# Kernel optimization log

Hardware: AMD Instinct MI355X
Metric: run time of the kernel (lower is better)

The kernel has to match this reference:

```python
import jax, jax.numpy as jnp
import numpy as np


def _rconv(x, w, b):
    # reflection-pad 1 then 3x3 valid conv (same spatial size), NCHW/OIHW
    xp = jnp.pad(x, ((0, 0), (0, 0), (1, 1), (1, 1)), mode='reflect')
    y = jax.lax.conv_general_dilated(
        xp, w, window_strides=(1, 1), padding='VALID',
        dimension_numbers=('NCHW', 'OIHW', 'NCHW'))
    return y + b[None, :, None, None]


def setup_inputs() -> dict:
    key = jax.random.key(0)
    ks = jax.random.split(key, 12)
    B, C, H, W = 4, 256, 64, 64
    IC = 128  # inter_channels
    s = lambda fan_in: 1.0 / np.sqrt(fan_in)
    return {
        'query_feat': jax.random.normal(ks[0], (B, C, H, W), jnp.float32),
        'key_feat': jax.random.normal(ks[1], (B, C, H, W), jnp.float32),
        # 1x1 conv projections (stored as [out, in])
        'w_theta': jax.random.normal(ks[2], (IC, C), jnp.float32) * s(C),
        'b_theta': jnp.zeros((IC,), jnp.float32),
        'w_phi': jax.random.normal(ks[3], (IC, C), jnp.float32) * s(C),
        'b_phi': jnp.zeros((IC,), jnp.float32),
        # post-correlation block: conv(1->32), residual(32), conv(32->1)
        'w_in': jax.random.normal(ks[4], (32, 1, 3, 3), jnp.float32) * s(9),
        'b_in': jnp.zeros((32,), jnp.float32),
        'w_r1': jax.random.normal(ks[5], (32, 32, 3, 3), jnp.float32) * s(32 * 9),
        'b_r1': jnp.zeros((32,), jnp.float32),
        'w_r2': jax.random.normal(ks[6], (32, 32, 3, 3), jnp.float32) * s(32 * 9),
        'b_r2': jnp.zeros((32,), jnp.float32),
        'w_out': jax.random.normal(ks[7], (1, 32, 3, 3), jnp.float32) * s(32 * 9),
        'b_out': jnp.zeros((1,), jnp.float32),
    }


def reference(query_feat, key_feat, w_theta, b_theta, w_phi, b_phi,
              w_in, b_in, w_r1, b_r1, w_r2, b_r2, w_out, b_out):
    B, C, H, W = query_feat.shape
    N = H * W
    # 1x1 conv projections, flattened to sequences
    theta = jnp.einsum('oc,bchw->bohw', w_theta, query_feat) + b_theta[None, :, None, None]
    phi = jnp.einsum('oc,bchw->bohw', w_phi, key_feat) + b_phi[None, :, None, None]
    theta = theta.reshape(B, -1, N).transpose(0, 2, 1)  # [B, N, IC]
    phi = phi.reshape(B, -1, N)                          # [B, IC, N]
    # correlation matrix [B, N, N] then max over key positions
    f = jnp.matmul(theta, phi)
    sim = jnp.max(f, axis=-1).reshape(B, 1, H, W)
    # post-correlation conv refinement
    h = _rconv(sim, w_in, b_in)                      # 1 -> 32
    r = jax.nn.relu(_rconv(h, w_r1, b_r1))           # residual block
    r = _rconv(r, w_r2, b_r2)
    h = h + r
    out = _rconv(h, w_out, b_out)                    # 32 -> 1
    return out
```

## Files before the change

### kernel.cpp

```cpp
#include <hip/hip_runtime.h>

#define B_ 4
#define C_ 256
#define HH 64
#define WW 64
#define N_ 4096
#define IC_ 128
#define JC_ 8

typedef __attribute__((ext_vector_type(8))) short bf16x8;
typedef __attribute__((ext_vector_type(4))) float f32x4;

__device__ __forceinline__ short f2bf(float f) {
    unsigned u = __builtin_bit_cast(unsigned, f);
    unsigned r = (u + 0x7FFFu + ((u >> 16) & 1u)) >> 16;
    return (short)r;
}

__device__ __forceinline__ int refl(int v) {
    return v < 0 ? -v : (v > 63 ? 126 - v : v);
}

__global__ __launch_bounds__(256) void k_cvt_w(const float* __restrict__ wt,
                                               const float* __restrict__ wp,
                                               short* __restrict__ wtb,
                                               short* __restrict__ wpb) {
    int i = blockIdx.x * 256 + threadIdx.x;
    wtb[i] = f2bf(wt[i]);
    wpb[i] = f2bf(wp[i]);
}

__global__ __launch_bounds__(256) void k_project(
    const float* __restrict__ qf, const float* __restrict__ kf,
    const short* __restrict__ wq, const short* __restrict__ wk,
    const float* __restrict__ bq, const float* __restrict__ bk,
    short* __restrict__ outq, short* __restrict__ outk) {
    int z = blockIdx.z;
    const float* x = z ? kf : qf;
    const short* wbf = z ? wk : wq;
    const float* bias = z ? bk : bq;
    short* outT = z ? outk : outq;

    int b = blockIdx.y;
    int n0 = blockIdx.x * 32;
    int t = threadIdx.x;
    int lane = t & 63, wv = t >> 6;
    int l15 = lane & 15, q4 = lane >> 4;
    const float* xb = x + (size_t)b * C_ * N_;

    __shared__ float xs[2][32][36];

    f32x4 acc[2][2];
#pragma unroll
    for (int rf = 0; rf < 2; rf++)
#pragma unroll
        for (int cfi = 0; cfi < 2; cfi++) acc[rf][cfi] = (f32x4){0.f, 0.f, 0.f, 0.f};

    int sr = t >> 3, sc = t & 7;
    *(f32x4*)(&xs[0][sr][sc * 4]) = *(const f32x4*)(xb + (size_t)sr * N_ + n0 + sc * 4);

    for (int ks = 0; ks < 8; ks++) {
        __syncthreads();
        int buf = ks & 1;
        if (ks < 7) {
            int cb = (ks + 1) * 32;
            *(f32x4*)(&xs[buf ^ 1][sr][sc * 4]) =
                *(const f32x4*)(xb + (size_t)(cb + sr) * N_ + n0 + sc * 4);
        }
        int cbase = ks * 32 + q4 * 8;
        bf16x8 a[2];
#pragma unroll
        for (int rf = 0; rf < 2; rf++)
#pragma unroll
            for (int j = 0; j < 8; j++) a[rf][j] = f2bf(xs[buf][q4 * 8 + j][rf * 16 + l15]);
#pragma unroll
        for (int cfi = 0; cfi < 2; cfi++) {
            int cf = wv * 2 + cfi;
            bf16x8 bfr = *(const bf16x8*)(wbf + (size_t)(cf * 16 + l15) * C_ + cbase);
#pragma unroll
            for (int rf = 0; rf < 2; rf++)
                acc[rf][cfi] = __builtin_amdgcn_mfma_f32_16x16x32_bf16(a[rf], bfr, acc[rf][cfi], 0, 0, 0);
        }
    }
#pragma unroll
    for (int cfi = 0; cfi < 2; cfi++) {
        int ic = (wv * 2 + cfi) * 16 + l15;
        float bv = bias[ic];
#pragma unroll
        for (int rf = 0; rf < 2; rf++) {
#pragma unroll
            for (int r = 0; r < 4; r++) {
                int n = n0 + rf * 16 + q4 * 4 + r;
                outT[((size_t)b * N_ + n) * IC_ + ic] = f2bf(acc[rf][cfi][r] + bv);
            }
        }
    }
}

__global__ __launch_bounds__(256, 4) void k_corr(const short* __restrict__ thetaT,
                                                 const short* __restrict__ phiT,
                                                 float* __restrict__ simp) {
    __shared__ short ph[2][64][136];

    int b = blockIdx.z, jc = blockIdx.y;
    int i0 = blockIdx.x * 128;
    int t = threadIdx.x;
    int lane = t & 63, w = t >> 6;
    int l15 = lane & 15, q4 = lane >> 4;

    const short* thb = thetaT + ((size_t)b * N_ + i0 + w * 32) * IC_;
    const short* phb = phiT + ((size_t)b * N_ + jc * (N_ / JC_)) * IC_;

    bf16x8 afr[2][4];
#pragma unroll
    for (int rf = 0; rf < 2; rf++)
#pragma unroll
        for (int ks = 0; ks < 4; ks++)
            afr[rf][ks] = *(const bf16x8*)(thb + (size_t)(rf * 16 + l15) * IC_ + ks * 32 + q4 * 8);

    int srow = t >> 4, sc8 = t & 15;
#pragma unroll
    for (int k = 0; k < 4; k++)
        *(bf16x8*)(&ph[0][srow + k * 16][sc8 * 8]) =
            *(const bf16x8*)(phb + (size_t)(srow + k * 16) * IC_ + sc8 * 8);

    f32x4 rmax[2];
#pragma unroll
    for (int rf = 0; rf < 2; rf++) rmax[rf] = (f32x4){-3.0e38f, -3.0e38f, -3.0e38f, -3.0e38f};

    const int NT = (N_ / JC_) / 64;
    for (int it = 0; it < NT; it++) {
        int buf = it & 1;
        __syncthreads();
        if (it < NT - 1) {
            int j0 = (it + 1) * 64;
#pragma unroll
            for (int k = 0; k < 4; k++)
                *(bf16x8*)(&ph[buf ^ 1][srow + k * 16][sc8 * 8]) =
                    *(const bf16x8*)(phb + (size_t)(j0 + srow + k * 16) * IC_ + sc8 * 8);
        }
#pragma unroll
        for (int jf = 0; jf < 4; jf++) {
            bf16x8 bfr[4];
#pragma unroll
            for (int ks = 0; ks < 4; ks++)
                bfr[ks] = *(const bf16x8*)(&ph[buf][jf * 16 + l15][ks * 32 + q4 * 8]);
#pragma unroll
            for (int rf = 0; rf < 2; rf++) {
                f32x4 a2 = (f32x4){0.f, 0.f, 0.f, 0.f};
#pragma unroll
                for (int ks = 0; ks < 4; ks++)
                    a2 = __builtin_amdgcn_mfma_f32_16x16x32_bf16(afr[rf][ks], bfr[ks], a2, 0, 0, 0);
#pragma unroll
                for (int r = 0; r < 4; r++) rmax[rf][r] = fmaxf(rmax[rf][r], a2[r]);
            }
        }
    }

#pragma unroll
    for (int rf = 0; rf < 2; rf++) {
#pragma unroll
        for (int r = 0; r < 4; r++) {
            float v = rmax[rf][r];
            v = fmaxf(v, __shfl_xor(v, 1));
            v = fmaxf(v, __shfl_xor(v, 2));
            v = fmaxf(v, __shfl_xor(v, 4));
            v = fmaxf(v, __shfl_xor(v, 8));
            rmax[rf][r] = v;
        }
    }
    if (l15 == 0) {
        float* sp = simp + ((size_t)(b * JC_ + jc)) * N_ + i0 + w * 32;
#pragma unroll
        for (int rf = 0; rf < 2; rf++)
#pragma unroll
            for (int r = 0; r < 4; r++) sp[rf * 16 + q4 * 4 + r] = rmax[rf][r];
    }
}

__global__ __launch_bounds__(256) void k_conv_in(const float* __restrict__ simp,
                                                 const float* __restrict__ w,
                                                 const float* __restrict__ bias,
                                                 float* __restrict__ h) {
    int y = blockIdx.x, b = blockIdx.y;
    int t = threadIdx.x;
    int oc = t >> 3, x8 = t & 7;
    __shared__ float srow[3][66];
    const float* sb = simp + (size_t)b * JC_ * N_;
    if (t < 192) {
        int r = t >> 6, x = t & 63;
        int idx = refl(y - 1 + r) * 64 + x;
        float v = -3.0e38f;
#pragma unroll
        for (int jc = 0; jc < JC_; jc++) v = fmaxf(v, sb[jc * N_ + idx]);
        srow[r][x + 1] = v;
    }
    if (t < 3) {
        int gy = refl(y - 1 + t);
        float vl = -3.0e38f, vr = -3.0e38f;
#pragma unroll
        for (int jc = 0; jc < JC_; jc++) {
            vl = fmaxf(vl, sb[jc * N_ + gy * 64 + 1]);
            vr = fmaxf(vr, sb[jc * N_ + gy * 64 + 62]);
        }
        srow[t][0] = vl;
        srow[t][65] = vr;
    }
    __syncthreads();

    float wr[9];
#pragma unroll
    for (int k = 0; k < 9; k++) wr[k] = w[oc * 9 + k];
    float bv = bias[oc];
    float acc[8];
#pragma unroll
    for (int xi = 0; xi < 8; xi++) acc[xi] = bv;
#pragma unroll
    for (int ky = 0; ky < 3; ky++)
#pragma unroll
        for (int kx = 0; kx < 3; kx++) {
            float wv2 = wr[ky * 3 + kx];
#pragma unroll
            for (int xi = 0; xi < 8; xi++) acc[xi] += wv2 * srow[ky][x8 * 8 + xi + kx];
        }
    float* op = h + (((size_t)b * 32 + oc) * 64 + y) * 64 + x8 * 8;
#pragma unroll
    for (int xi = 0; xi < 8; xi++) op[xi] = acc[xi];
}

template <bool RELU, bool ADD>
__global__ __launch_bounds__(256) void k_conv_r(const float* __restrict__ in,
                                                const float* __restrict__ w,
                                                const float* __restrict__ bias,
                                                float* __restrict__ out,
                                                const float* __restrict__ add) {
    int y = blockIdx.x, b = blockIdx.z;
    int oc0 = blockIdx.y * 16;
    int t = threadIdx.x;
    __shared__ float tile[32][3][68];
    __shared__ float wlds[32 * 16 * 12];

#pragma unroll
    for (int k = 0; k < 18; k++) {
        int id = t + k * 256;
        int ocl = id / 288;
        int rem = id - ocl * 288;
        int ic = rem / 9;
        int tap = rem - ic * 9;
        wlds[(ic * 16 + ocl) * 12 + tap] = w[(size_t)(oc0 + ocl) * 288 + rem];
    }

#pragma unroll
    for (int r = 0; r < 3; r++) {
        int gy = refl(y - 1 + r);
#pragma unroll
        for (int i = 0; i < 2; i++) {
            int idx = t + i * 256;
            int ic = idx >> 4, c4 = idx & 15;
            f32x4 v = *(const f32x4*)(in + (((size_t)b * 32 + ic) * 64 + gy) * 64 + c4 * 4);
#pragma unroll
            for (int s = 0; s < 4; s++) tile[ic][r][c4 * 4 + s + 1] = v[s];
        }
    }
    if (t < 96) {
        int ic = t / 3, r = t - ic * 3;
        int gy = refl(y - 1 + r);
        const float* row = in + (((size_t)b * 32 + ic) * 64 + gy) * 64;
        tile[ic][r][0] = row[1];
        tile[ic][r][65] = row[62];
    }
    __syncthreads();

    int ocl = t >> 4, x4 = (t & 15) * 4;
    float bv = bias[oc0 + ocl];
    float acc[4];
#pragma unroll
    for (int xi = 0; xi < 4; xi++) acc[xi] = bv;

#pragma unroll 2
    for (int ic = 0; ic < 32; ic++) {
        const float* wr = &wlds[(ic * 16 + ocl) * 12];
        f32x4 W0 = *(const f32x4*)(wr);
        f32x4 W1 = *(const f32x4*)(wr + 4);
        f32x4 W2 = *(const f32x4*)(wr + 8);
        float w0 = W0[0], w1 = W0[1], w2 = W0[2], w3 = W0[3];
        float w4 = W1[0], w5 = W1[1], w6 = W1[2], w7 = W1[3];
        float w8 = W2[0];
        float xr[3][8];
#pragma unroll
        for (int r = 0; r < 3; r++) {
            const float* rowp = &tile[ic][r][x4];
            f32x4 A = *(const f32x4*)(rowp);
            f32x4 Bv = *(const f32x4*)(rowp + 4);
            xr[r][0] = A[0]; xr[r][1] = A[1]; xr[r][2] = A[2]; xr[r][3] = A[3];
            xr[r][4] = Bv[0]; xr[r][5] = Bv[1]; xr[r][6] = Bv[2]; xr[r][7] = Bv[3];
        }
#pragma unroll
        for (int xi = 0; xi < 4; xi++) {
            acc[xi] += w0 * xr[0][xi] + w1 * xr[0][xi + 1] + w2 * xr[0][xi + 2] +
                       w3 * xr[1][xi] + w4 * xr[1][xi + 1] + w5 * xr[1][xi + 2] +
                       w6 * xr[2][xi] + w7 * xr[2][xi + 1] + w8 * xr[2][xi + 2];
        }
    }
    size_t off = (((size_t)b * 32 + oc0 + ocl) * 64 + y) * 64 + x4;
#pragma unroll
    for (int xi = 0; xi < 4; xi++) {
        float v = acc[xi];
        if (RELU) v = fmaxf(v, 0.f);
        if (ADD) v += add[off + xi];
        out[off + xi] = v;
    }
}

__global__ __launch_bounds__(256) void k_conv_out(const float* __restrict__ hb,
                                                  const float* __restrict__ w,
                                                  const float* __restrict__ bias,
                                                  float* __restrict__ outp) {
    int y = blockIdx.x, b = blockIdx.y;
    int t = threadIdx.x;
    int x = t & 63, g = t >> 6;
    __shared__ float red[4][64];
    __shared__ float wl[288];
    for (int k = t; k < 288; k += 256) wl[k] = w[k];
    __syncthreads();
    float acc = 0.f;
#pragma unroll
    for (int i = 0; i < 8; i++) {
        int ic = g * 8 + i;
        const float* wp = wl + ic * 9;
#pragma unroll
        for (int ky = 0; ky < 3; ky++) {
            int gy = refl(y + ky - 1);
            const float* row = hb + (((size_t)b * 32 + ic) * 64 + gy) * 64;
#pragma unroll
            for (int kx = 0; kx < 3; kx++) {
                int gx = refl(x + kx - 1);
                acc += wp[ky * 3 + kx] * row[gx];
            }
        }
    }
    red[g][x] = acc;
    __syncthreads();
    if (t < 64) {
        outp[((size_t)b * 64 + y) * 64 + x] =
            bias[0] + red[0][t] + red[1][t] + red[2][t] + red[3][t];
    }
}

extern "C" void kernel_launch(void* const* d_in, const int* in_sizes, int n_in,
                              void* d_out, int out_size, void* d_ws, size_t ws_size,
                              hipStream_t stream) {
    const float* q = (const float*)d_in[0];
    const float* kf = (const float*)d_in[1];
    const float* w_theta = (const float*)d_in[2];
    const float* b_theta = (const float*)d_in[3];
    const float* w_phi = (const float*)d_in[4];
    const float* b_phi = (const float*)d_in[5];
    const float* w_in = (const float*)d_in[6];
    const float* b_in = (const float*)d_in[7];
    const float* w_r1 = (const float*)d_in[8];
    const float* b_r1 = (const float*)d_in[9];
    const float* w_r2 = (const float*)d_in[10];
    const float* b_r2 = (const float*)d_in[11];
    const float* w_out = (const float*)d_in[12];
    const float* b_out = (const float*)d_in[13];
    float* out = (float*)d_out;

    char* ws = (char*)d_ws;
    short* thetaT = (short*)(ws);
    short* phiT = (short*)(ws + 4194304);
    short* wthb = (short*)(ws + 8388608);
    short* wphb = (short*)(ws + 8454144);
    float* simp = (float*)(ws + 8519680);
    float* h = (float*)(ws);
    float* r = (float*)(ws + 2097152);

    k_cvt_w<<<128, 256, 0, stream>>>(w_theta, w_phi, wthb, wphb);
    k_project<<<dim3(128, 4, 2), 256, 0, stream>>>(q, kf, wthb, wphb, b_theta, b_phi,
                                                   thetaT, phiT);
    k_corr<<<dim3(32, JC_, 4), 256, 0, stream>>>(thetaT, phiT, simp);
    k_conv_in<<<dim3(64, 4), 256, 0, stream>>>(simp, w_in, b_in, h);
    k_conv_r<true, false><<<dim3(64, 2, 4), 256, 0, stream>>>(h, w_r1, b_r1, r, nullptr);
    k_conv_r<false, true><<<dim3(64, 2, 4), 256, 0, stream>>>(r, w_r2, b_r2, h, h);
    k_conv_out<<<dim3(64, 4), 256, 0, stream>>>(h, w_out, b_out, out);
}
```

Before: 166.9 us.

## Fuse weight conversion and conv_in into neighbors; double rows per corr block

Drops the separate weight bf16 conversion kernel: the projection kernel now reads fp32 weights and rounds them in registers. The correlation kernel handles 256 query rows per block instead of 128, so each LDS phi tile feeds twice as many MFMAs, at the cost of more registers (launch bound lowered to 2) and half as many blocks. The first 1->32 conv is fused into the first residual conv: each block recomputes h over a 3-row halo from the partial-max buffer, and one y-slice of blocks writes h out. Two launches go away in exchange for some redundant conv_in work.

```diff
diff --git a/kernel.cpp b/kernel.cpp
--- a/kernel.cpp
+++ b/kernel.cpp
@@ -21,23 +21,14 @@
     return v < 0 ? -v : (v > 63 ? 126 - v : v);
 }
 
-__global__ __launch_bounds__(256) void k_cvt_w(const float* __restrict__ wt,
-                                               const float* __restrict__ wp,
-                                               short* __restrict__ wtb,
-                                               short* __restrict__ wpb) {
-    int i = blockIdx.x * 256 + threadIdx.x;
-    wtb[i] = f2bf(wt[i]);
-    wpb[i] = f2bf(wp[i]);
-}
-
 __global__ __launch_bounds__(256) void k_project(
     const float* __restrict__ qf, const float* __restrict__ kf,
-    const short* __restrict__ wq, const short* __restrict__ wk,
+    const float* __restrict__ wq, const float* __restrict__ wk,
     const float* __restrict__ bq, const float* __restrict__ bk,
     short* __restrict__ outq, short* __restrict__ outk) {
     int z = blockIdx.z;
     const float* x = z ? kf : qf;
-    const short* wbf = z ? wk : wq;
+    const float* wf = z ? wk : wq;
     const float* bias = z ? bk : bq;
     short* outT = z ? outk : outq;
 
@@ -76,7 +67,15 @@
 #pragma unroll
         for (int cfi = 0; cfi < 2; cfi++) {
             int cf = wv * 2 + cfi;
-            bf16x8 bfr = *(const bf16x8*)(wbf + (size_t)(cf * 16 + l15) * C_ + cbase);
+            const float* wrow = wf + (size_t)(cf * 16 + l15) * C_ + cbase;
+            f32x4 w0 = *(const f32x4*)(wrow);
+            f32x4 w1 = *(const f32x4*)(wrow + 4);
+            bf16x8 bfr;
+#pragma unroll
+            for (int j = 0; j < 4; j++) {
+                bfr[j] = f2bf(w0[j]);
+                bfr[j + 4] = f2bf(w1[j]);
+            }
 #pragma unroll
             for (int rf = 0; rf < 2; rf++)
                 acc[rf][cfi] = __builtin_amdgcn_mfma_f32_16x16x32_bf16(a[rf], bfr, acc[rf][cfi], 0, 0, 0);
@@ -97,36 +96,36 @@
     }
 }
 
-__global__ __launch_bounds__(256, 4) void k_corr(const short* __restrict__ thetaT,
+__global__ __launch_bounds__(256, 2) void k_corr(const short* __restrict__ thetaT,
                                                  const short* __restrict__ phiT,
                                                  float* __restrict__ simp) {
     __shared__ short ph[2][64][136];
 
     int b = blockIdx.z, jc = blockIdx.y;
-    int i0 = blockIdx.x * 128;
+    int i0 = blockIdx.x * 256;
     int t = threadIdx.x;
     int lane = t & 63, w = t >> 6;
     int l15 = lane & 15, q4 = lane >> 4;
 
-    const short* thb = thetaT + ((size_t)b * N_ + i0 + w * 32) * IC_;
+    const short* thb = thetaT + ((size_t)b * N_ + i0 + w * 64) * IC_;
     const short* phb = phiT + ((size_t)b * N_ + jc * (N_ / JC_)) * IC_;
 
-    bf16x8 afr[2][4];
-#pragma unroll
-    for (int rf = 0; rf < 2; rf++)
+    bf16x8 afr[4][4];
+#pragma unroll
+    for (int rf = 0; rf < 4; rf++)
 #pragma unroll
         for (int ks = 0; ks < 4; ks++)
             afr[rf][ks] = *(const bf16x8*)(thb + (size_t)(rf * 16 + l15) * IC_ + ks * 32 + q4 * 8);
 
-    int srow = t >> 4, sc8 = t & 15;
+    int sr = t >> 4, sc8 = t & 15;
 #pragma unroll
     for (int k = 0; k < 4; k++)
-        *(bf16x8*)(&ph[0][srow + k * 16][sc8 * 8]) =
-            *(const bf16x8*)(phb + (size_t)(srow + k * 16) * IC_ + sc8 * 8);
-
-    f32x4 rmax[2];
-#pragma unroll
-    for (int rf = 0; rf < 2; rf++) rmax[rf] = (f32x4){-3.0e38f, -3.0e38f, -3.0e38f, -3.0e38f};
+        *(bf16x8*)(&ph[0][sr + k * 16][sc8 * 8]) =
+            *(const bf16x8*)(phb + (size_t)(sr + k * 16) * IC_ + sc8 * 8);
+
+    f32x4 rmax[4];
+#pragma unroll
+    for (int rf = 0; rf < 4; rf++) rmax[rf] = (f32x4){-3.0e38f, -3.0e38f, -3.0e38f, -3.0e38f};
 
     const int NT = (N_ / JC_) / 64;
     for (int it = 0; it < NT; it++) {
@@ -136,8 +135,8 @@
             int j0 = (it + 1) * 64;
 #pragma unroll
             for (int k = 0; k < 4; k++)
-                *(bf16x8*)(&ph[buf ^ 1][srow + k * 16][sc8 * 8]) =
-                    *(const bf16x8*)(phb + (size_t)(j0 + srow + k * 16) * IC_ + sc8 * 8);
+                *(bf16x8*)(&ph[buf ^ 1][sr + k * 16][sc8 * 8]) =
+                    *(const bf16x8*)(phb + (size_t)(j0 + sr + k * 16) * IC_ + sc8 * 8);
         }
 #pragma unroll
         for (int jf = 0; jf < 4; jf++) {
@@ -146,7 +145,7 @@
             for (int ks = 0; ks < 4; ks++)
                 bfr[ks] = *(const bf16x8*)(&ph[buf][jf * 16 + l15][ks * 32 + q4 * 8]);
 #pragma unroll
-            for (int rf = 0; rf < 2; rf++) {
+            for (int rf = 0; rf < 4; rf++) {
                 f32x4 a2 = (f32x4){0.f, 0.f, 0.f, 0.f};
 #pragma unroll
                 for (int ks = 0; ks < 4; ks++)
@@ -158,7 +157,7 @@
     }
 
 #pragma unroll
-    for (int rf = 0; rf < 2; rf++) {
+    for (int rf = 0; rf < 4; rf++) {
 #pragma unroll
         for (int r = 0; r < 4; r++) {
             float v = rmax[rf][r];
@@ -170,62 +169,128 @@
         }
     }
     if (l15 == 0) {
-        float* sp = simp + ((size_t)(b * JC_ + jc)) * N_ + i0 + w * 32;
-#pragma unroll
-        for (int rf = 0; rf < 2; rf++)
+        float* sp = simp + ((size_t)(b * JC_ + jc)) * N_ + i0 + w * 64;
+#pragma unroll
+        for (int rf = 0; rf < 4; rf++)
 #pragma unroll
             for (int r = 0; r < 4; r++) sp[rf * 16 + q4 * 4 + r] = rmax[rf][r];
     }
 }
 
-__global__ __launch_bounds__(256) void k_conv_in(const float* __restrict__ simp,
-                                                 const float* __restrict__ w,
-                                                 const float* __restrict__ bias,
-                                                 float* __restrict__ h) {
-    int y = blockIdx.x, b = blockIdx.y;
+__global__ __launch_bounds__(256) void k_r1_fused(
+    const float* __restrict__ simp,
+    const float* __restrict__ win, const float* __restrict__ bin,
+    const float* __restrict__ w, const float* __restrict__ bias,
+    float* __restrict__ rout, float* __restrict__ hout) {
+    int y = blockIdx.x, b = blockIdx.z;
+    int oc0 = blockIdx.y * 16;
     int t = threadIdx.x;
-    int oc = t >> 3, x8 = t & 7;
-    __shared__ float srow[3][66];
+    __shared__ float srow[5][66];
+    __shared__ float tile[32][3][68];
+    __shared__ float wlds[32 * 16 * 12];
+    __shared__ float wi[288];
+    __shared__ float bi[32];
+
+    for (int k = t; k < 288; k += 256) wi[k] = win[k];
+    if (t < 32) bi[t] = bin[t];
+
     const float* sb = simp + (size_t)b * JC_ * N_;
-    if (t < 192) {
-        int r = t >> 6, x = t & 63;
-        int idx = refl(y - 1 + r) * 64 + x;
+    for (int idx = t; idx < 330; idx += 256) {
+        int d = idx / 66, cc = idx - d * 66;
+        int row = refl(y - 2 + d);
+        int col = refl(cc - 1);
         float v = -3.0e38f;
 #pragma unroll
-        for (int jc = 0; jc < JC_; jc++) v = fmaxf(v, sb[jc * N_ + idx]);
-        srow[r][x + 1] = v;
-    }
-    if (t < 3) {
-        int gy = refl(y - 1 + t);
-        float vl = -3.0e38f, vr = -3.0e38f;
-#pragma unroll
-        for (int jc = 0; jc < JC_; jc++) {
-            vl = fmaxf(vl, sb[jc * N_ + gy * 64 + 1]);
-            vr = fmaxf(vr, sb[jc * N_ + gy * 64 + 62]);
-        }
-        srow[t][0] = vl;
-        srow[t][65] = vr;
+        for (int jc = 0; jc < JC_; jc++) v = fmaxf(v, sb[jc * N_ + row * 64 + col]);
+        srow[d][cc] = v;
+    }
+
+#pragma unroll
+    for (int k = 0; k < 18; k++) {
+        int id = t + k * 256;
+        int ocl = id / 288;
+        int rem = id - ocl * 288;
+        int ic = rem / 9;
+        int tap = rem - ic * 9;
+        wlds[(ic * 16 + ocl) * 12 + tap] = w[(size_t)(oc0 + ocl) * 288 + rem];
     }
     __syncthreads();
 
-    float wr[9];
-#pragma unroll
-    for (int k = 0; k < 9; k++) wr[k] = w[oc * 9 + k];
-    float bv = bias[oc];
-    float acc[8];
-#pragma unroll
-    for (int xi = 0; xi < 8; xi++) acc[xi] = bv;
-#pragma unroll
-    for (int ky = 0; ky < 3; ky++)
-#pragma unroll
-        for (int kx = 0; kx < 3; kx++) {
-            float wv2 = wr[ky * 3 + kx];
-#pragma unroll
-            for (int xi = 0; xi < 8; xi++) acc[xi] += wv2 * srow[ky][x8 * 8 + xi + kx];
-        }
-    float* op = h + (((size_t)b * 32 + oc) * 64 + y) * 64 + x8 * 8;
-#pragma unroll
-    for (int xi = 0; xi < 8; xi++) op[xi] = acc[xi];
+    {
+        int ic = t >> 3, xg = t & 7;
+        float bv = bi[ic];
+        float wr[9];
+#pragma unroll
+        for (int k2 = 0; k2 < 9; k2++) wr[k2] = wi[ic * 9 + k2];
+#pragma unroll
+        for (int r = 0; r < 3; r++) {
+            int gy = refl(y - 1 + r);
+            int s0 = refl(gy - 1) - y + 2;
+            int s1 = gy - y + 2;
+            int s2 = refl(gy + 1) - y + 2;
+#pragma unroll
+            for (int k2 = 0; k2 < 9; k2++) {
+                int xs = k2 * 8 + xg;
+                if (xs < 66) {
+                    int cp = refl(xs - 1);
+                    float a = bv;
+                    a += wr[0] * srow[s0][cp];
+                    a += wr[1] * srow[s0][cp + 1];
+                    a += wr[2] * srow[s0][cp + 2];
+                    a += wr[3] * srow[s1][cp];
+                    a += wr[4] * srow[s1][cp + 1];
+                    a += wr[5] * srow[s1][cp + 2];
+                    a += wr[6] * srow[s2][cp];
+                    a += wr[7] * srow[s2][cp + 1];
+                    a += wr[8] * srow[s2][cp + 2];
+                    tile[ic][r][xs] = a;
+                }
+            }
+        }
+    }
+    __syncthreads();
+
+    if (blockIdx.y == 0) {
+        for (int idx = t; idx < 2048; idx += 256) {
+            int ic = idx >> 6, x = idx & 63;
+            hout[(((size_t)b * 32 + ic) * 64 + y) * 64 + x] = tile[ic][1][x + 1];
+        }
+    }
+
+    int ocl = t >> 4, x4 = (t & 15) * 4;
+    float bv = bias[oc0 + ocl];
+    float acc[4];
+#pragma unroll
+    for (int xi = 0; xi < 4; xi++) acc[xi] = bv;
+
+#pragma unroll 2
+    for (int ic = 0; ic < 32; ic++) {
+        const float* wr = &wlds[(ic * 16 + ocl) * 12];
+        f32x4 W0 = *(const f32x4*)(wr);
+        f32x4 W1 = *(const f32x4*)(wr + 4);
+        f32x4 W2 = *(const f32x4*)(wr + 8);
+        float w0 = W0[0], w1 = W0[1], w2 = W0[2], w3 = W0[3];
+        float w4 = W1[0], w5 = W1[1], w6 = W1[2], w7 = W1[3];
+        float w8 = W2[0];
+        float xr[3][8];
+#pragma unroll
+        for (int r = 0; r < 3; r++) {
+            const float* rowp = &tile[ic][r][x4];
+            f32x4 A = *(const f32x4*)(rowp);
+            f32x4 Bv = *(const f32x4*)(rowp + 4);
+            xr[r][0] = A[0]; xr[r][1] = A[1]; xr[r][2] = A[2]; xr[r][3] = A[3];
+            xr[r][4] = Bv[0]; xr[r][5] = Bv[1]; xr[r][6] = Bv[2]; xr[r][7] = Bv[3];
+        }
+#pragma unroll
+        for (int xi = 0; xi < 4; xi++) {
+            acc[xi] += w0 * xr[0][xi] + w1 * xr[0][xi + 1] + w2 * xr[0][xi + 2] +
+                       w3 * xr[1][xi] + w4 * xr[1][xi + 1] + w5 * xr[1][xi + 2] +
+                       w6 * xr[2][xi] + w7 * xr[2][xi + 1] + w8 * xr[2][xi + 2];
+        }
+    }
+    size_t off = (((size_t)b * 32 + oc0 + ocl) * 64 + y) * 64 + x4;
+#pragma unroll
+    for (int xi = 0; xi < 4; xi++) rout[off + xi] = fmaxf(acc[xi], 0.f);
 }
 
 template <bool RELU, bool ADD>
@@ -369,18 +434,14 @@
     char* ws = (char*)d_ws;
     short* thetaT = (short*)(ws);
     short* phiT = (short*)(ws + 4194304);
-    short* wthb = (short*)(ws + 8388608);
-    short* wphb = (short*)(ws + 8454144);
     float* simp = (float*)(ws + 8519680);
     float* h = (float*)(ws);
     float* r = (float*)(ws + 2097152);
 
-    k_cvt_w<<<128, 256, 0, stream>>>(w_theta, w_phi, wthb, wphb);
-    k_project<<<dim3(128, 4, 2), 256, 0, stream>>>(q, kf, wthb, wphb, b_theta, b_phi,
+    k_project<<<dim3(128, 4, 2), 256, 0, stream>>>(q, kf, w_theta, w_phi, b_theta, b_phi,
                                                    thetaT, phiT);
-    k_corr<<<dim3(32, JC_, 4), 256, 0, stream>>>(thetaT, phiT, simp);
-    k_conv_in<<<dim3(64, 4), 256, 0, stream>>>(simp, w_in, b_in, h);
-    k_conv_r<true, false><<<dim3(64, 2, 4), 256, 0, stream>>>(h, w_r1, b_r1, r, nullptr);
+    k_corr<<<dim3(16, JC_, 4), 256, 0, stream>>>(thetaT, phiT, simp);
+    k_r1_fused<<<dim3(64, 2, 4), 256, 0, stream>>>(simp, w_in, b_in, w_r1, b_r1, r, h);
     k_conv_r<false, true><<<dim3(64, 2, 4), 256, 0, stream>>>(r, w_r2, b_r2, h, h);
     k_conv_out<<<dim3(64, 4), 256, 0, stream>>>(h, w_out, b_out, out);
 }
```

Measured after the change: 171.3 us. +2.6%, slower.

## Fuse post-correlation conv chain into one cooperative kernel with grid syncs

Applied to the files above, without the earlier changes.

Replaces the four separate conv launches (conv_in, two residual convs, conv_out) with a single cooperative kernel of 256 blocks that uses grid-wide syncs between stages. The aim is to remove per-launch overhead and inter-kernel gaps. It also drops the separate weight-conversion kernel and converts the projection weights to bf16 inside the projection kernel. In exchange, each block handles both output-channel halves serially, and grid.sync carries its own cost. The old launches are kept as a fallback if the cooperative launch fails.

```diff
diff --git a/kernel.cpp b/kernel.cpp
--- a/kernel.cpp
+++ b/kernel.cpp
@@ -1,4 +1,7 @@
 #include <hip/hip_runtime.h>
+#include <hip/hip_cooperative_groups.h>
+
+namespace cg = cooperative_groups;
 
 #define B_ 4
 #define C_ 256
@@ -21,23 +24,14 @@
     return v < 0 ? -v : (v > 63 ? 126 - v : v);
 }
 
-__global__ __launch_bounds__(256) void k_cvt_w(const float* __restrict__ wt,
-                                               const float* __restrict__ wp,
-                                               short* __restrict__ wtb,
-                                               short* __restrict__ wpb) {
-    int i = blockIdx.x * 256 + threadIdx.x;
-    wtb[i] = f2bf(wt[i]);
-    wpb[i] = f2bf(wp[i]);
-}
-
 __global__ __launch_bounds__(256) void k_project(
     const float* __restrict__ qf, const float* __restrict__ kf,
-    const short* __restrict__ wq, const short* __restrict__ wk,
+    const float* __restrict__ wq, const float* __restrict__ wk,
     const float* __restrict__ bq, const float* __restrict__ bk,
     short* __restrict__ outq, short* __restrict__ outk) {
     int z = blockIdx.z;
     const float* x = z ? kf : qf;
-    const short* wbf = z ? wk : wq;
+    const float* wf = z ? wk : wq;
     const float* bias = z ? bk : bq;
     short* outT = z ? outk : outq;
 
@@ -76,7 +70,15 @@
 #pragma unroll
         for (int cfi = 0; cfi < 2; cfi++) {
             int cf = wv * 2 + cfi;
-            bf16x8 bfr = *(const bf16x8*)(wbf + (size_t)(cf * 16 + l15) * C_ + cbase);
+            const float* wrow = wf + (size_t)(cf * 16 + l15) * C_ + cbase;
+            f32x4 w0 = *(const f32x4*)(wrow);
+            f32x4 w1 = *(const f32x4*)(wrow + 4);
+            bf16x8 bfr;
+#pragma unroll
+            for (int j = 0; j < 4; j++) {
+                bfr[j] = f2bf(w0[j]);
+                bfr[j + 4] = f2bf(w1[j]);
+            }
 #pragma unroll
             for (int rf = 0; rf < 2; rf++)
                 acc[rf][cfi] = __builtin_amdgcn_mfma_f32_16x16x32_bf16(a[rf], bfr, acc[rf][cfi], 0, 0, 0);
@@ -175,6 +177,204 @@
         for (int rf = 0; rf < 2; rf++)
 #pragma unroll
             for (int r = 0; r < 4; r++) sp[rf * 16 + q4 * 4 + r] = rmax[rf][r];
+    }
+}
+
+__device__ __forceinline__ void stage_tile32(const float* in, int b, int y, int t,
+                                             float (*tile)[3][68]) {
+#pragma unroll
+    for (int r = 0; r < 3; r++) {
+        int gy = refl(y - 1 + r);
+#pragma unroll
+        for (int i = 0; i < 2; i++) {
+            int idx = t + i * 256;
+            int ic = idx >> 4, c4 = idx & 15;
+            f32x4 v = *(const f32x4*)(in + (((size_t)b * 32 + ic) * 64 + gy) * 64 + c4 * 4);
+#pragma unroll
+            for (int s = 0; s < 4; s++) tile[ic][r][c4 * 4 + s + 1] = v[s];
+        }
+    }
+    if (t < 96) {
+        int ic = t / 3, r = t - ic * 3;
+        int gy = refl(y - 1 + r);
+        const float* row = in + (((size_t)b * 32 + ic) * 64 + gy) * 64;
+        tile[ic][r][0] = row[1];
+        tile[ic][r][65] = row[62];
+    }
+}
+
+__device__ __forceinline__ void load_wlds(const float* wg, int oc0, int t, float* wlds) {
+#pragma unroll
+    for (int k = 0; k < 18; k++) {
+        int id = t + k * 256;
+        int ocl = id / 288;
+        int rem = id - ocl * 288;
+        int ic = rem / 9;
+        int tap = rem - ic * 9;
+        wlds[(ic * 16 + ocl) * 12 + tap] = wg[(size_t)(oc0 + ocl) * 288 + rem];
+    }
+}
+
+template <bool RELU, bool ADD>
+__device__ __forceinline__ void conv32_compute(const float* bias, float* outp,
+                                               const float* addp, int y, int oc0, int b,
+                                               int t, const float (*tile)[3][68],
+                                               const float* wlds) {
+    int ocl = t >> 4, x4 = (t & 15) * 4;
+    float bv = bias[oc0 + ocl];
+    float acc[4];
+#pragma unroll
+    for (int xi = 0; xi < 4; xi++) acc[xi] = bv;
+
+#pragma unroll 2
+    for (int ic = 0; ic < 32; ic++) {
+        const float* wr = &wlds[(ic * 16 + ocl) * 12];
+        f32x4 W0 = *(const f32x4*)(wr);
+        f32x4 W1 = *(const f32x4*)(wr + 4);
+        f32x4 W2 = *(const f32x4*)(wr + 8);
+        float w0 = W0[0], w1 = W0[1], w2 = W0[2], w3 = W0[3];
+        float w4 = W1[0], w5 = W1[1], w6 = W1[2], w7 = W1[3];
+        float w8 = W2[0];
+        float xr[3][8];
+#pragma unroll
+        for (int r = 0; r < 3; r++) {
+            const float* rowp = &tile[ic][r][x4];
+            f32x4 A = *(const f32x4*)(rowp);
+            f32x4 Bv = *(const f32x4*)(rowp + 4);
+            xr[r][0] = A[0]; xr[r][1] = A[1]; xr[r][2] = A[2]; xr[r][3] = A[3];
+            xr[r][4] = Bv[0]; xr[r][5] = Bv[1]; xr[r][6] = Bv[2]; xr[r][7] = Bv[3];
+        }
+#pragma unroll
+        for (int xi = 0; xi < 4; xi++) {
+            acc[xi] += w0 * xr[0][xi] + w1 * xr[0][xi + 1] + w2 * xr[0][xi + 2] +
+                       w3 * xr[1][xi] + w4 * xr[1][xi + 1] + w5 * xr[1][xi + 2] +
+                       w6 * xr[2][xi] + w7 * xr[2][xi + 1] + w8 * xr[2][xi + 2];
+        }
+    }
+    size_t off = (((size_t)b * 32 + oc0 + ocl) * 64 + y) * 64 + x4;
+#pragma unroll
+    for (int xi = 0; xi < 4; xi++) {
+        float v = acc[xi];
+        if (RELU) v = fmaxf(v, 0.f);
+        if (ADD) v += addp[off + xi];
+        outp[off + xi] = v;
+    }
+}
+
+__global__ __launch_bounds__(256) void k_tail(
+    const float* __restrict__ simp,
+    const float* __restrict__ win, const float* __restrict__ bin,
+    const float* __restrict__ w1, const float* __restrict__ b1,
+    const float* __restrict__ w2, const float* __restrict__ b2,
+    const float* __restrict__ wo, const float* __restrict__ bo,
+    float* h, float* r, float* outp) {
+    cg::grid_group grid = cg::this_grid();
+    int t = threadIdx.x;
+    int bid = blockIdx.x;
+    int y = bid & 63, b = bid >> 6;
+
+    __shared__ float srow[3][66];
+    __shared__ float tile[32][3][68];
+    __shared__ float wlds[32 * 16 * 12];
+    __shared__ float wsm[288];
+    __shared__ float bsm[32];
+    __shared__ float red[4][64];
+
+    {
+        int oc = t >> 3, x8 = t & 7;
+        const float* sb = simp + (size_t)b * JC_ * N_;
+        for (int k = t; k < 288; k += 256) wsm[k] = win[k];
+        if (t < 32) bsm[t] = bin[t];
+        if (t < 192) {
+            int rr = t >> 6, x = t & 63;
+            int idx = refl(y - 1 + rr) * 64 + x;
+            float v = -3.0e38f;
+#pragma unroll
+            for (int jc = 0; jc < JC_; jc++) v = fmaxf(v, sb[jc * N_ + idx]);
+            srow[rr][x + 1] = v;
+        }
+        if (t < 3) {
+            int gy = refl(y - 1 + t);
+            float vl = -3.0e38f, vr = -3.0e38f;
+#pragma unroll
+            for (int jc = 0; jc < JC_; jc++) {
+                vl = fmaxf(vl, sb[jc * N_ + gy * 64 + 1]);
+                vr = fmaxf(vr, sb[jc * N_ + gy * 64 + 62]);
+            }
+            srow[t][0] = vl;
+            srow[t][65] = vr;
+        }
+        __syncthreads();
+        float wr[9];
+#pragma unroll
+        for (int k = 0; k < 9; k++) wr[k] = wsm[oc * 9 + k];
+        float bv = bsm[oc];
+        float acc[8];
+#pragma unroll
+        for (int xi = 0; xi < 8; xi++) acc[xi] = bv;
+#pragma unroll
+        for (int ky = 0; ky < 3; ky++)
+#pragma unroll
+            for (int kx = 0; kx < 3; kx++) {
+                float wv2 = wr[ky * 3 + kx];
+#pragma unroll
+                for (int xi = 0; xi < 8; xi++) acc[xi] += wv2 * srow[ky][x8 * 8 + xi + kx];
+            }
+        float* op = h + (((size_t)b * 32 + oc) * 64 + y) * 64 + x8 * 8;
+#pragma unroll
+        for (int xi = 0; xi < 8; xi++) op[xi] = acc[xi];
+    }
+    __threadfence();
+    grid.sync();
+
+    stage_tile32(h, b, y, t, tile);
+#pragma unroll
+    for (int oh = 0; oh < 2; oh++) {
+        load_wlds(w1, oh * 16, t, wlds);
+        __syncthreads();
+        conv32_compute<true, false>(b1, r, nullptr, y, oh * 16, b, t, tile, wlds);
+        __syncthreads();
+    }
+    __threadfence();
+    grid.sync();
+
+    stage_tile32(r, b, y, t, tile);
+#pragma unroll
+    for (int oh = 0; oh < 2; oh++) {
+        load_wlds(w2, oh * 16, t, wlds);
+        __syncthreads();
+        conv32_compute<false, true>(b2, h, h, y, oh * 16, b, t, tile, wlds);
+        __syncthreads();
+    }
+    __threadfence();
+    grid.sync();
+
+    {
+        int x = t & 63, g = t >> 6;
+        for (int k = t; k < 288; k += 256) wsm[k] = wo[k];
+        __syncthreads();
+        float acc = 0.f;
+#pragma unroll
+        for (int i = 0; i < 8; i++) {
+            int ic = g * 8 + i;
+            const float* wp = wsm + ic * 9;
+#pragma unroll
+            for (int ky = 0; ky < 3; ky++) {
+                int gy = refl(y + ky - 1);
+                const float* row = h + (((size_t)b * 32 + ic) * 64 + gy) * 64;
+#pragma unroll
+                for (int kx = 0; kx < 3; kx++) {
+                    int gx = refl(x + kx - 1);
+                    acc += wp[ky * 3 + kx] * row[gx];
+                }
+            }
+        }
+        red[g][x] = acc;
+        __syncthreads();
+        if (t < 64) {
+            outp[((size_t)b * 64 + y) * 64 + x] =
+                bo[0] + red[0][t] + red[1][t] + red[2][t] + red[3][t];
+        }
     }
 }
 
@@ -186,7 +386,9 @@
     int t = threadIdx.x;
     int oc = t >> 3, x8 = t & 7;
     __shared__ float srow[3][66];
+    __shared__ float wsm[288];
     const float* sb = simp + (size_t)b * JC_ * N_;
+    for (int k = t; k < 288; k += 256) wsm[k] = w[k];
     if (t < 192) {
         int r = t >> 6, x = t & 63;
         int idx = refl(y - 1 + r) * 64 + x;
@@ -210,7 +412,7 @@
 
     float wr[9];
 #pragma unroll
-    for (int k = 0; k < 9; k++) wr[k] = w[oc * 9 + k];
+    for (int k = 0; k < 9; k++) wr[k] = wsm[oc * 9 + k];
     float bv = bias[oc];
     float acc[8];
 #pragma unroll
@@ -239,77 +441,10 @@
     int t = threadIdx.x;
     __shared__ float tile[32][3][68];
     __shared__ float wlds[32 * 16 * 12];
-
-#pragma unroll
-    for (int k = 0; k < 18; k++) {
-        int id = t + k * 256;
-        int ocl = id / 288;
-        int rem = id - ocl * 288;
-        int ic = rem / 9;
-        int tap = rem - ic * 9;
-        wlds[(ic * 16 + ocl) * 12 + tap] = w[(size_t)(oc0 + ocl) * 288 + rem];
-    }
-
-#pragma unroll
-    for (int r = 0; r < 3; r++) {
-        int gy = refl(y - 1 + r);
-#pragma unroll
-        for (int i = 0; i < 2; i++) {
-            int idx = t + i * 256;
-            int ic = idx >> 4, c4 = idx & 15;
-            f32x4 v = *(const f32x4*)(in + (((size_t)b * 32 + ic) * 64 + gy) * 64 + c4 * 4);
-#pragma unroll
-            for (int s = 0; s < 4; s++) tile[ic][r][c4 * 4 + s + 1] = v[s];
-        }
-    }
-    if (t < 96) {
-        int ic = t / 3, r = t - ic * 3;
-        int gy = refl(y - 1 + r);
-        const float* row = in + (((size_t)b * 32 + ic) * 64 + gy) * 64;
-        tile[ic][r][0] = row[1];
-        tile[ic][r][65] = row[62];
-    }
+    load_wlds(w, oc0, t, wlds);
+    stage_tile32(in, b, y, t, tile);
     __syncthreads();
-
-    int ocl = t >> 4, x4 = (t & 15) * 4;
-    float bv = bias[oc0 + ocl];
-    float acc[4];
-#pragma unroll
-    for (int xi = 0; xi < 4; xi++) acc[xi] = bv;
-
-#pragma unroll 2
-    for (int ic = 0; ic < 32; ic++) {
-        const float* wr = &wlds[(ic * 16 + ocl) * 12];
-        f32x4 W0 = *(const f32x4*)(wr);
-        f32x4 W1 = *(const f32x4*)(wr + 4);
-        f32x4 W2 = *(const f32x4*)(wr + 8);
-        float w0 = W0[0], w1 = W0[1], w2 = W0[2], w3 = W0[3];
-        float w4 = W1[0], w5 = W1[1], w6 = W1[2], w7 = W1[3];
-        float w8 = W2[0];
-        float xr[3][8];
-#pragma unroll
-        for (int r = 0; r < 3; r++) {
-            const float* rowp = &tile[ic][r][x4];
-            f32x4 A = *(const f32x4*)(rowp);
-            f32x4 Bv = *(const f32x4*)(rowp + 4);
-            xr[r][0] = A[0]; xr[r][1] = A[1]; xr[r][2] = A[2]; xr[r][3] = A[3];
-            xr[r][4] = Bv[0]; xr[r][5] = Bv[1]; xr[r][6] = Bv[2]; xr[r][7] = Bv[3];
-        }
-#pragma unroll
-        for (int xi = 0; xi < 4; xi++) {
-            acc[xi] += w0 * xr[0][xi] + w1 * xr[0][xi + 1] + w2 * xr[0][xi + 2] +
-                       w3 * xr[1][xi] + w4 * xr[1][xi + 1] + w5 * xr[1][xi + 2] +
-                       w6 * xr[2][xi] + w7 * xr[2][xi + 1] + w8 * xr[2][xi + 2];
-        }
-    }
-    size_t off = (((size_t)b * 32 + oc0 + ocl) * 64 + y) * 64 + x4;
-#pragma unroll
-    for (int xi = 0; xi < 4; xi++) {
-        float v = acc[xi];
-        if (RELU) v = fmaxf(v, 0.f);
-        if (ADD) v += add[off + xi];
-        out[off + xi] = v;
-    }
+    conv32_compute<RELU, ADD>(bias, out, add, y, oc0, b, t, tile, wlds);
 }
 
 __global__ __launch_bounds__(256) void k_conv_out(const float* __restrict__ hb,
@@ -369,18 +504,30 @@
     char* ws = (char*)d_ws;
     short* thetaT = (short*)(ws);
     short* phiT = (short*)(ws + 4194304);
-    short* wthb = (short*)(ws + 8388608);
-    short* wphb = (short*)(ws + 8454144);
     float* simp = (float*)(ws + 8519680);
     float* h = (float*)(ws);
     float* r = (float*)(ws + 2097152);
 
-    k_cvt_w<<<128, 256, 0, stream>>>(w_theta, w_phi, wthb, wphb);
-    k_project<<<dim3(128, 4, 2), 256, 0, stream>>>(q, kf, wthb, wphb, b_theta, b_phi,
+    k_project<<<dim3(128, 4, 2), 256, 0, stream>>>(q, kf, w_theta, w_phi, b_theta, b_phi,
                                                    thetaT, phiT);
     k_corr<<<dim3(32, JC_, 4), 256, 0, stream>>>(thetaT, phiT, simp);
-    k_conv_in<<<dim3(64, 4), 256, 0, stream>>>(simp, w_in, b_in, h);
-    k_conv_r<true, false><<<dim3(64, 2, 4), 256, 0, stream>>>(h, w_r1, b_r1, r, nullptr);
-    k_conv_r<false, true><<<dim3(64, 2, 4), 256, 0, stream>>>(r, w_r2, b_r2, h, h);
-    k_conv_out<<<dim3(64, 4), 256, 0, stream>>>(h, w_out, b_out, out);
-}
+
+    {
+        const float* simp_c = simp;
+        float* hp = h;
+        float* rp = r;
+        float* op = out;
+        void* args[] = {(void*)&simp_c, (void*)&w_in, (void*)&b_in,
+                        (void*)&w_r1,   (void*)&b_r1, (void*)&w_r2, (void*)&b_r2,
+                        (void*)&w_out,  (void*)&b_out,
+                        (void*)&hp,     (void*)&rp,   (void*)&op};
+        hipError_t e = hipLaunchCooperativeKernel((const void*)k_tail, dim3(256),
+                                                  dim3(256), (void**)args, 0, stream);
+        if (e != hipSuccess) {
+            k_conv_in<<<dim3(64, 4), 256, 0, stream>>>(simp, w_in, b_in, h);
+            k_conv_r<true, false><<<dim3(64, 2, 4), 256, 0, stream>>>(h, w_r1, b_r1, r, nullptr);
+            k_conv_r<false, true><<<dim3(64, 2, 4), 256, 0, stream>>>(r, w_r2, b_r2, h, h);
+            k_conv_out<<<dim3(64, 4), 256, 0, stream>>>(h, w_out, b_out, out);
+        }
+    }
+}
```

Result: slower. 362.3 us (+117.1%).

## Fuse weight bf16 conversion into projection and enlarge correlation row tile

Applied to the files above, without the earlier changes.

Drops the separate weight-conversion kernel: the projection kernel now reads fp32 weights and converts them to bf16 in registers, saving one launch. The correlation kernel doubles its query rows per block (64 per wave, 256 per block), so each phi tile staged in LDS feeds twice as many MFMAs, and the grid halves. Occupancy is lowered to 2 blocks per CU to leave room for the larger register footprint. The conv kernels are refactored into helpers, and conv_in now stages its weights in shared memory.

```diff
diff --git a/kernel.cpp b/kernel.cpp
--- a/kernel.cpp
+++ b/kernel.cpp
@@ -21,23 +21,14 @@
     return v < 0 ? -v : (v > 63 ? 126 - v : v);
 }
 
-__global__ __launch_bounds__(256) void k_cvt_w(const float* __restrict__ wt,
-                                               const float* __restrict__ wp,
-                                               short* __restrict__ wtb,
-                                               short* __restrict__ wpb) {
-    int i = blockIdx.x * 256 + threadIdx.x;
-    wtb[i] = f2bf(wt[i]);
-    wpb[i] = f2bf(wp[i]);
-}
-
 __global__ __launch_bounds__(256) void k_project(
     const float* __restrict__ qf, const float* __restrict__ kf,
-    const short* __restrict__ wq, const short* __restrict__ wk,
+    const float* __restrict__ wq, const float* __restrict__ wk,
     const float* __restrict__ bq, const float* __restrict__ bk,
     short* __restrict__ outq, short* __restrict__ outk) {
     int z = blockIdx.z;
     const float* x = z ? kf : qf;
-    const short* wbf = z ? wk : wq;
+    const float* wf = z ? wk : wq;
     const float* bias = z ? bk : bq;
     short* outT = z ? outk : outq;
 
@@ -76,7 +67,15 @@
 #pragma unroll
         for (int cfi = 0; cfi < 2; cfi++) {
             int cf = wv * 2 + cfi;
-            bf16x8 bfr = *(const bf16x8*)(wbf + (size_t)(cf * 16 + l15) * C_ + cbase);
+            const float* wrow = wf + (size_t)(cf * 16 + l15) * C_ + cbase;
+            f32x4 w0 = *(const f32x4*)(wrow);
+            f32x4 w1 = *(const f32x4*)(wrow + 4);
+            bf16x8 bfr;
+#pragma unroll
+            for (int j = 0; j < 4; j++) {
+                bfr[j] = f2bf(w0[j]);
+                bfr[j + 4] = f2bf(w1[j]);
+            }
 #pragma unroll
             for (int rf = 0; rf < 2; rf++)
                 acc[rf][cfi] = __builtin_amdgcn_mfma_f32_16x16x32_bf16(a[rf], bfr, acc[rf][cfi], 0, 0, 0);
@@ -97,36 +96,36 @@
     }
 }
 
-__global__ __launch_bounds__(256, 4) void k_corr(const short* __restrict__ thetaT,
+__global__ __launch_bounds__(256, 2) void k_corr(const short* __restrict__ thetaT,
                                                  const short* __restrict__ phiT,
                                                  float* __restrict__ simp) {
     __shared__ short ph[2][64][136];
 
     int b = blockIdx.z, jc = blockIdx.y;
-    int i0 = blockIdx.x * 128;
+    int i0 = blockIdx.x * 256;
     int t = threadIdx.x;
     int lane = t & 63, w = t >> 6;
     int l15 = lane & 15, q4 = lane >> 4;
 
-    const short* thb = thetaT + ((size_t)b * N_ + i0 + w * 32) * IC_;
+    const short* thb = thetaT + ((size_t)b * N_ + i0 + w * 64) * IC_;
     const short* phb = phiT + ((size_t)b * N_ + jc * (N_ / JC_)) * IC_;
 
-    bf16x8 afr[2][4];
-#pragma unroll
-    for (int rf = 0; rf < 2; rf++)
+    bf16x8 afr[4][4];
+#pragma unroll
+    for (int rf = 0; rf < 4; rf++)
 #pragma unroll
         for (int ks = 0; ks < 4; ks++)
             afr[rf][ks] = *(const bf16x8*)(thb + (size_t)(rf * 16 + l15) * IC_ + ks * 32 + q4 * 8);
 
-    int srow = t >> 4, sc8 = t & 15;
+    int sr = t >> 4, sc8 = t & 15;
 #pragma unroll
     for (int k = 0; k < 4; k++)
-        *(bf16x8*)(&ph[0][srow + k * 16][sc8 * 8]) =
-            *(const bf16x8*)(phb + (size_t)(srow + k * 16) * IC_ + sc8 * 8);
-
-    f32x4 rmax[2];
-#pragma unroll
-    for (int rf = 0; rf < 2; rf++) rmax[rf] = (f32x4){-3.0e38f, -3.0e38f, -3.0e38f, -3.0e38f};
+        *(bf16x8*)(&ph[0][sr + k * 16][sc8 * 8]) =
+            *(const bf16x8*)(phb + (size_t)(sr + k * 16) * IC_ + sc8 * 8);
+
+    f32x4 rmax[4];
+#pragma unroll
+    for (int rf = 0; rf < 4; rf++) rmax[rf] = (f32x4){-3.0e38f, -3.0e38f, -3.0e38f, -3.0e38f};
 
     const int NT = (N_ / JC_) / 64;
     for (int it = 0; it < NT; it++) {
@@ -136,8 +135,8 @@
             int j0 = (it + 1) * 64;
 #pragma unroll
             for (int k = 0; k < 4; k++)
-                *(bf16x8*)(&ph[buf ^ 1][srow + k * 16][sc8 * 8]) =
-                    *(const bf16x8*)(phb + (size_t)(j0 + srow + k * 16) * IC_ + sc8 * 8);
+                *(bf16x8*)(&ph[buf ^ 1][sr + k * 16][sc8 * 8]) =
+                    *(const bf16x8*)(phb + (size_t)(j0 + sr + k * 16) * IC_ + sc8 * 8);
         }
 #pragma unroll
         for (int jf = 0; jf < 4; jf++) {
@@ -146,7 +145,7 @@
             for (int ks = 0; ks < 4; ks++)
                 bfr[ks] = *(const bf16x8*)(&ph[buf][jf * 16 + l15][ks * 32 + q4 * 8]);
 #pragma unroll
-            for (int rf = 0; rf < 2; rf++) {
+            for (int rf = 0; rf < 4; rf++) {
                 f32x4 a2 = (f32x4){0.f, 0.f, 0.f, 0.f};
 #pragma unroll
                 for (int ks = 0; ks < 4; ks++)
@@ -158,7 +157,7 @@
     }
 
 #pragma unroll
-    for (int rf = 0; rf < 2; rf++) {
+    for (int rf = 0; rf < 4; rf++) {
 #pragma unroll
         for (int r = 0; r < 4; r++) {
             float v = rmax[rf][r];
@@ -170,76 +169,38 @@
         }
     }
     if (l15 == 0) {
-        float* sp = simp + ((size_t)(b * JC_ + jc)) * N_ + i0 + w * 32;
-#pragma unroll
-        for (int rf = 0; rf < 2; rf++)
+        float* sp = simp + ((size_t)(b * JC_ + jc)) * N_ + i0 + w * 64;
+#pragma unroll
+        for (int rf = 0; rf < 4; rf++)
 #pragma unroll
             for (int r = 0; r < 4; r++) sp[rf * 16 + q4 * 4 + r] = rmax[rf][r];
     }
 }
 
-__global__ __launch_bounds__(256) void k_conv_in(const float* __restrict__ simp,
-                                                 const float* __restrict__ w,
-                                                 const float* __restrict__ bias,
-                                                 float* __restrict__ h) {
-    int y = blockIdx.x, b = blockIdx.y;
-    int t = threadIdx.x;
-    int oc = t >> 3, x8 = t & 7;
-    __shared__ float srow[3][66];
-    const float* sb = simp + (size_t)b * JC_ * N_;
-    if (t < 192) {
-        int r = t >> 6, x = t & 63;
-        int idx = refl(y - 1 + r) * 64 + x;
-        float v = -3.0e38f;
-#pragma unroll
-        for (int jc = 0; jc < JC_; jc++) v = fmaxf(v, sb[jc * N_ + idx]);
-        srow[r][x + 1] = v;
-    }
-    if (t < 3) {
-        int gy = refl(y - 1 + t);
-        float vl = -3.0e38f, vr = -3.0e38f;
-#pragma unroll
-        for (int jc = 0; jc < JC_; jc++) {
-            vl = fmaxf(vl, sb[jc * N_ + gy * 64 + 1]);
-            vr = fmaxf(vr, sb[jc * N_ + gy * 64 + 62]);
-        }
-        srow[t][0] = vl;
-        srow[t][65] = vr;
-    }
-    __syncthreads();
-
-    float wr[9];
-#pragma unroll
-    for (int k = 0; k < 9; k++) wr[k] = w[oc * 9 + k];
-    float bv = bias[oc];
-    float acc[8];
-#pragma unroll
-    for (int xi = 0; xi < 8; xi++) acc[xi] = bv;
-#pragma unroll
-    for (int ky = 0; ky < 3; ky++)
-#pragma unroll
-        for (int kx = 0; kx < 3; kx++) {
-            float wv2 = wr[ky * 3 + kx];
-#pragma unroll
-            for (int xi = 0; xi < 8; xi++) acc[xi] += wv2 * srow[ky][x8 * 8 + xi + kx];
-        }
-    float* op = h + (((size_t)b * 32 + oc) * 64 + y) * 64 + x8 * 8;
-#pragma unroll
-    for (int xi = 0; xi < 8; xi++) op[xi] = acc[xi];
-}
-
-template <bool RELU, bool ADD>
-__global__ __launch_bounds__(256) void k_conv_r(const float* __restrict__ in,
-                                                const float* __restrict__ w,
-                                                const float* __restrict__ bias,
-                                                float* __restrict__ out,
-                                                const float* __restrict__ add) {
-    int y = blockIdx.x, b = blockIdx.z;
-    int oc0 = blockIdx.y * 16;
-    int t = threadIdx.x;
-    __shared__ float tile[32][3][68];
-    __shared__ float wlds[32 * 16 * 12];
-
+__device__ __forceinline__ void stage_tile32(const float* in, int b, int y, int t,
+                                             float (*tile)[3][68]) {
+#pragma unroll
+    for (int r = 0; r < 3; r++) {
+        int gy = refl(y - 1 + r);
+#pragma unroll
+        for (int i = 0; i < 2; i++) {
+            int idx = t + i * 256;
+            int ic = idx >> 4, c4 = idx & 15;
+            f32x4 v = *(const f32x4*)(in + (((size_t)b * 32 + ic) * 64 + gy) * 64 + c4 * 4);
+#pragma unroll
+            for (int s = 0; s < 4; s++) tile[ic][r][c4 * 4 + s + 1] = v[s];
+        }
+    }
+    if (t < 96) {
+        int ic = t / 3, r = t - ic * 3;
+        int gy = refl(y - 1 + r);
+        const float* row = in + (((size_t)b * 32 + ic) * 64 + gy) * 64;
+        tile[ic][r][0] = row[1];
+        tile[ic][r][65] = row[62];
+    }
+}
+
+__device__ __forceinline__ void load_wlds(const float* wg, int oc0, int t, float* wlds) {
 #pragma unroll
     for (int k = 0; k < 18; k++) {
         int id = t + k * 256;
@@ -247,30 +208,15 @@
         int rem = id - ocl * 288;
         int ic = rem / 9;
         int tap = rem - ic * 9;
-        wlds[(ic * 16 + ocl) * 12 + tap] = w[(size_t)(oc0 + ocl) * 288 + rem];
-    }
-
-#pragma unroll
-    for (int r = 0; r < 3; r++) {
-        int gy = refl(y - 1 + r);
-#pragma unroll
-        for (int i = 0; i < 2; i++) {
-            int idx = t + i * 256;
-            int ic = idx >> 4, c4 = idx & 15;
-            f32x4 v = *(const f32x4*)(in + (((size_t)b * 32 + ic) * 64 + gy) * 64 + c4 * 4);
-#pragma unroll
-            for (int s = 0; s < 4; s++) tile[ic][r][c4 * 4 + s + 1] = v[s];
-        }
-    }
-    if (t < 96) {
-        int ic = t / 3, r = t - ic * 3;
-        int gy = refl(y - 1 + r);
-        const float* row = in + (((size_t)b * 32 + ic) * 64 + gy) * 64;
-        tile[ic][r][0] = row[1];
-        tile[ic][r][65] = row[62];
-    }
-    __syncthreads();
-
+        wlds[(ic * 16 + ocl) * 12 + tap] = wg[(size_t)(oc0 + ocl) * 288 + rem];
+    }
+}
+
+template <bool RELU, bool ADD>
+__device__ __forceinline__ void conv32_compute(const float* bias, float* outp,
+                                               const float* addp, int y, int oc0, int b,
+                                               int t, const float (*tile)[3][68],
+                                               const float* wlds) {
     int ocl = t >> 4, x4 = (t & 15) * 4;
     float bv = bias[oc0 + ocl];
     float acc[4];
@@ -307,9 +253,78 @@
     for (int xi = 0; xi < 4; xi++) {
         float v = acc[xi];
         if (RELU) v = fmaxf(v, 0.f);
-        if (ADD) v += add[off + xi];
-        out[off + xi] = v;
-    }
+        if (ADD) v += addp[off + xi];
+        outp[off + xi] = v;
+    }
+}
+
+__global__ __launch_bounds__(256) void k_conv_in(const float* __restrict__ simp,
+                                                 const float* __restrict__ w,
+                                                 const float* __restrict__ bias,
+                                                 float* __restrict__ h) {
+    int y = blockIdx.x, b = blockIdx.y;
+    int t = threadIdx.x;
+    int oc = t >> 3, x8 = t & 7;
+    __shared__ float srow[3][66];
+    __shared__ float wsm[288];
+    const float* sb = simp + (size_t)b * JC_ * N_;
+    for (int k = t; k < 288; k += 256) wsm[k] = w[k];
+    if (t < 192) {
+        int r = t >> 6, x = t & 63;
+        int idx = refl(y - 1 + r) * 64 + x;
+        float v = -3.0e38f;
+#pragma unroll
+        for (int jc = 0; jc < JC_; jc++) v = fmaxf(v, sb[jc * N_ + idx]);
+        srow[r][x + 1] = v;
+    }
+    if (t < 3) {
+        int gy = refl(y - 1 + t);
+        float vl = -3.0e38f, vr = -3.0e38f;
+#pragma unroll
+        for (int jc = 0; jc < JC_; jc++) {
+            vl = fmaxf(vl, sb[jc * N_ + gy * 64 + 1]);
+            vr = fmaxf(vr, sb[jc * N_ + gy * 64 + 62]);
+        }
+        srow[t][0] = vl;
+        srow[t][65] = vr;
+    }
+    __syncthreads();
+
+    float wr[9];
+#pragma unroll
+    for (int k = 0; k < 9; k++) wr[k] = wsm[oc * 9 + k];
+    float bv = bias[oc];
+    float acc[8];
+#pragma unroll
+    for (int xi = 0; xi < 8; xi++) acc[xi] = bv;
+#pragma unroll
+    for (int ky = 0; ky < 3; ky++)
+#pragma unroll
+        for (int kx = 0; kx < 3; kx++) {
+            float wv2 = wr[ky * 3 + kx];
+#pragma unroll
+            for (int xi = 0; xi < 8; xi++) acc[xi] += wv2 * srow[ky][x8 * 8 + xi + kx];
+        }
+    float* op = h + (((size_t)b * 32 + oc) * 64 + y) * 64 + x8 * 8;
+#pragma unroll
+    for (int xi = 0; xi < 8; xi++) op[xi] = acc[xi];
+}
+
+template <bool RELU, bool ADD>
+__global__ __launch_bounds__(256) void k_conv_r(const float* __restrict__ in,
+                                                const float* __restrict__ w,
+                                                const float* __restrict__ bias,
+                                                float* __restrict__ out,
+                                                const float* __restrict__ add) {
+    int y = blockIdx.x, b = blockIdx.z;
+    int oc0 = blockIdx.y * 16;
+    int t = threadIdx.x;
+    __shared__ float tile[32][3][68];
+    __shared__ float wlds[32 * 16 * 12];
+    load_wlds(w, oc0, t, wlds);
+    stage_tile32(in, b, y, t, tile);
+    __syncthreads();
+    conv32_compute<RELU, ADD>(bias, out, add, y, oc0, b, t, tile, wlds);
 }
 
 __global__ __launch_bounds__(256) void k_conv_out(const float* __restrict__ hb,
@@ -369,16 +384,13 @@
     char* ws = (char*)d_ws;
     short* thetaT = (short*)(ws);
     short* phiT = (short*)(ws + 4194304);
-    short* wthb = (short*)(ws + 8388608);
-    short* wphb = (short*)(ws + 8454144);
     float* simp = (float*)(ws + 8519680);
     float* h = (float*)(ws);
     float* r = (float*)(ws + 2097152);
 
-    k_cvt_w<<<128, 256, 0, stream>>>(w_theta, w_phi, wthb, wphb);
-    k_project<<<dim3(128, 4, 2), 256, 0, stream>>>(q, kf, wthb, wphb, b_theta, b_phi,
+    k_project<<<dim3(128, 4, 2), 256, 0, stream>>>(q, kf, w_theta, w_phi, b_theta, b_phi,
                                                    thetaT, phiT);
-    k_corr<<<dim3(32, JC_, 4), 256, 0, stream>>>(thetaT, phiT, simp);
+    k_corr<<<dim3(16, JC_, 4), 256, 0, stream>>>(thetaT, phiT, simp);
     k_conv_in<<<dim3(64, 4), 256, 0, stream>>>(simp, w_in, b_in, h);
     k_conv_r<true, false><<<dim3(64, 2, 4), 256, 0, stream>>>(h, w_r1, b_r1, r, nullptr);
     k_conv_r<false, true><<<dim3(64, 2, 4), 256, 0, stream>>>(r, w_r2, b_r2, h, h);
```

Measured after the change: 171.2 us. 1.03x slower.
